# Kernel tuning notes

Hardware: AMD Instinct MI355X
Metric: run time of the kernel (lower is better)

Reference implementation:

```python
import jax, jax.numpy as jnp
import numpy as np

HEADS = 4
DIM_HEAD = 32
IN_CHANNELS = 256
SCALE = DIM_HEAD ** -0.5
EPS = 1e-5


def setup_inputs() -> dict:
    key = jax.random.key(0)
    ks = jax.random.split(key, 6)
    B, C, H, W = 16, IN_CHANNELS, 64, 64
    inner = HEADS * DIM_HEAD  # 128
    x = jax.random.normal(ks[0], (B, C, H, W), dtype=jnp.float32)
    # 1x1 conv weights are [out_ch, in_ch] (kernel spatial dims are 1)
    w_qkv = jax.random.normal(ks[1], (3 * inner, C), dtype=jnp.float32) * (C ** -0.5)
    w_out = jax.random.normal(ks[2], (C, inner), dtype=jnp.float32) * (inner ** -0.5)
    b_out = jax.random.normal(ks[3], (C,), dtype=jnp.float32) * 0.01
    gn_gamma = jnp.ones((C,), dtype=jnp.float32)
    gn_beta = jnp.zeros((C,), dtype=jnp.float32)
    return {"x": x, "w_qkv": w_qkv, "w_out": w_out, "b_out": b_out,
            "gn_gamma": gn_gamma, "gn_beta": gn_beta}


def reference(x, w_qkv, w_out, b_out, gn_gamma, gn_beta):
    b, c, h, w = x.shape
    n = h * w
    inner = HEADS * DIM_HEAD
    # 1x1 conv (no bias): [b, 3*inner, h, w], then chunk into q,k,v along channels
    qkv = jnp.einsum('oc,bchw->bohw', w_qkv, x)
    qkv = qkv.reshape(b, 3, HEADS, DIM_HEAD, n)  # chunk + 'b (h c) x y -> b h c (x y)'
    q, k, v = qkv[:, 0], qkv[:, 1], qkv[:, 2]    # each [b, heads, dim_head, n]
    q = jax.nn.softmax(q, axis=-2) * SCALE       # softmax over dim_head axis
    k = jax.nn.softmax(k, axis=-1)               # softmax over spatial axis
    context = jnp.einsum('bhdn,bhen->bhde', k, v)  # [b, heads, d, e]
    out = jnp.einsum('bhde,bhdn->bhen', context, q)  # [b, heads, e, n]
    out = out.reshape(b, inner, h, w)            # 'b h c (x y) -> b (h c) x y'
    # out 1x1 conv with bias
    out = jnp.einsum('oc,bchw->bohw', w_out, out) + b_out[None, :, None, None]
    # GroupNorm(num_groups=1): normalize over (C,H,W) per sample, per-channel affine
    mean = jnp.mean(out, axis=(1, 2, 3), keepdims=True)
    var = jnp.var(out, axis=(1, 2, 3), keepdims=True)
    out = (out - mean) * jax.lax.rsqrt(var + EPS)
    return out * gn_gamma[None, :, None, None] + gn_beta[None, :, None, None]
```

## Files before the change

### kernel.cpp

```cpp
#include <hip/hip_runtime.h>
#include <hip/hip_bf16.h>
#include <math.h>

#define B_SZ 16
#define C_IN 256
#define HEADS 4
#define DHEAD 32
#define INNER 128
#define QKV_CH 384
#define N_PIX 4096
#define SCALE_Q 0.17677669529663687f
#define GN_EPS 1e-5f
#define NCHK 32

typedef __attribute__((ext_vector_type(8))) short s16x8;
typedef __attribute__((ext_vector_type(4))) float f32x4;
typedef __attribute__((ext_vector_type(8))) unsigned short u16x8;
typedef __attribute__((ext_vector_type(4))) unsigned short u16x4;

__device__ __forceinline__ float waveSum(float v) {
#pragma unroll
  for (int off = 32; off > 0; off >>= 1) v += __shfl_down(v, off, 64);
  return v;
}
__device__ __forceinline__ unsigned short f2bf(float f) {
  unsigned int u = __builtin_bit_cast(unsigned int, f);
  unsigned int r = 0x7FFFu + ((u >> 16) & 1u);
  return (unsigned short)((u + r) >> 16);
}
__device__ __forceinline__ float bf2f(unsigned short u) {
  unsigned int x = ((unsigned int)u) << 16;
  return __builtin_bit_cast(float, x);
}

__global__ __launch_bounds__(256) void cvt_w(const float* __restrict__ wq,
                                             const float* __restrict__ wo,
                                             unsigned short* __restrict__ wqb,
                                             unsigned short* __restrict__ wob) {
  const int i = blockIdx.x * 256 + threadIdx.x;
  if (i < QKV_CH * C_IN) wqb[i] = f2bf(wq[i]);
  if (i < C_IN * INNER) wob[i] = f2bf(wo[i]);
}

__global__ __launch_bounds__(256) void qkv_gemm(const unsigned short* __restrict__ A,
                                                const float* __restrict__ X,
                                                unsigned short* __restrict__ Out) {
  const int b = blockIdx.y;
  const int n0 = blockIdx.x * 128;
  const int tid = threadIdx.x;
  const int w = tid >> 6, l = tid & 63;
  const int lr = l & 15, kg = l >> 4;
  const int mOff = (w >> 1) * 64, nOff = (w & 1) * 64;

  __shared__ unsigned short As[8192];
  __shared__ unsigned short Bs[32768];

  const float* xb = X + (size_t)b * C_IN * N_PIX;
  const int cq = tid >> 4, nq = tid & 15;

  for (int kc = 0; kc < C_IN; kc += 64) {
    float xr[8][4];
#pragma unroll
    for (int ci = 0; ci < 4; ++ci) {
      const float* xp = xb + (size_t)(kc + cq * 4 + ci) * N_PIX + n0 + nq;
#pragma unroll
      for (int k = 0; k < 8; ++k) xr[k][ci] = xp[k * 16];
    }
    const int c0b = (kc + cq * 4) * 2;
#pragma unroll
    for (int k = 0; k < 8; ++k) {
      const int row = nq + k * 16;
      u16x4 w4;
#pragma unroll
      for (int ci = 0; ci < 4; ++ci) w4[ci] = f2bf(xr[k][ci]);
      *reinterpret_cast<u16x4*>((char*)Bs + row * 512 + (c0b ^ ((row & 7) << 4))) = w4;
    }
  }

  unsigned short* Ob = Out + (size_t)b * QKV_CH * N_PIX;

  for (int mt = 0; mt < 3; ++mt) {
    const int m0 = mt * 128;
    f32x4 acc[4][4] = {};
    for (int kc = 0; kc < C_IN; kc += 64) {
#pragma unroll
      for (int s = 0; s < 4; ++s) {
        const int blk = (w * 4 + s) * 64 + l;
        const int r = blk >> 3;
        const int c = ((blk & 7) ^ (r & 7)) << 3;
        __builtin_amdgcn_global_load_lds(
            (const __attribute__((address_space(1))) void*)(A + (size_t)(m0 + r) * C_IN + kc + c),
            (__attribute__((address_space(3))) void*)((char*)As + (w * 4 + s) * 1024), 16, 0, 0);
      }
      __syncthreads();
#pragma unroll
      for (int ks = 0; ks < 2; ++ks) {
        const int kbyteA = ks * 64 + kg * 16;
        const int kbyteB = (kc + ks * 32 + kg * 8) * 2;
        s16x8 av[4], bv[4];
#pragma unroll
        for (int i = 0; i < 4; ++i) {
          const int row = mOff + i * 16 + lr;
          av[i] = *reinterpret_cast<const s16x8*>(
              (const char*)As + row * 128 + (kbyteA ^ ((row & 7) << 4)));
        }
#pragma unroll
        for (int j = 0; j < 4; ++j) {
          const int row = nOff + j * 16 + lr;
          bv[j] = *reinterpret_cast<const s16x8*>(
              (const char*)Bs + row * 512 + (kbyteB ^ ((row & 7) << 4)));
        }
#pragma unroll
        for (int i = 0; i < 4; ++i)
#pragma unroll
          for (int j = 0; j < 4; ++j)
            acc[i][j] = __builtin_amdgcn_mfma_f32_16x16x32_bf16(av[i], bv[j], acc[i][j], 0, 0, 0);
      }
      __syncthreads();
    }
#pragma unroll
    for (int i = 0; i < 4; ++i) {
      const int rowb = m0 + mOff + i * 16 + kg * 4;
#pragma unroll
      for (int j = 0; j < 4; ++j) {
        const int col = n0 + nOff + j * 16 + lr;
#pragma unroll
        for (int r = 0; r < 4; ++r)
          Ob[(size_t)(rowb + r) * N_PIX + col] = f2bf(acc[i][j][r]);
      }
    }
  }
}

__global__ __launch_bounds__(256) void ctx_mfma(const unsigned short* __restrict__ qkv,
                                                float* __restrict__ ctxp,
                                                float* __restrict__ mpart,
                                                float* __restrict__ spart) {
  const int wid = blockIdx.x * 4 + (threadIdx.x >> 6);
  const int l = threadIdx.x & 63;
  const int b = wid >> 7;
  const int h = (wid >> 5) & 3;
  const int c = wid & 31;
  const int lr = l & 15, kg = l >> 4;
  const unsigned short* kb =
      qkv + ((size_t)b * QKV_CH + INNER + h * DHEAD) * N_PIX + c * 128 + kg * 8;
  const unsigned short* vb = kb + (size_t)INNER * N_PIX;

  u16x8 kf[2][4], vf[2][4];
#pragma unroll
  for (int dt = 0; dt < 2; ++dt)
#pragma unroll
    for (int ks = 0; ks < 4; ++ks) {
      kf[dt][ks] = *reinterpret_cast<const u16x8*>(kb + (size_t)(dt * 16 + lr) * N_PIX + ks * 32);
      vf[dt][ks] = *reinterpret_cast<const u16x8*>(vb + (size_t)(dt * 16 + lr) * N_PIX + ks * 32);
    }
  float kv[2][4][8];
  float m[2] = {-INFINITY, -INFINITY};
#pragma unroll
  for (int dt = 0; dt < 2; ++dt)
#pragma unroll
    for (int ks = 0; ks < 4; ++ks)
#pragma unroll
      for (int j = 0; j < 8; ++j) {
        kv[dt][ks][j] = bf2f(kf[dt][ks][j]);
        m[dt] = fmaxf(m[dt], kv[dt][ks][j]);
      }
#pragma unroll
  for (int dt = 0; dt < 2; ++dt) {
    m[dt] = fmaxf(m[dt], __shfl_xor(m[dt], 16, 64));
    m[dt] = fmaxf(m[dt], __shfl_xor(m[dt], 32, 64));
  }
  float s[2] = {0.f, 0.f};
  s16x8 ka[2][4];
#pragma unroll
  for (int dt = 0; dt < 2; ++dt)
#pragma unroll
    for (int ks = 0; ks < 4; ++ks)
#pragma unroll
      for (int j = 0; j < 8; ++j) {
        const float e = __expf(kv[dt][ks][j] - m[dt]);
        s[dt] += e;
        ka[dt][ks][j] = (short)f2bf(e);
      }
#pragma unroll
  for (int dt = 0; dt < 2; ++dt) {
    s[dt] += __shfl_xor(s[dt], 16, 64);
    s[dt] += __shfl_xor(s[dt], 32, 64);
  }
  f32x4 acc[2][2] = {};
#pragma unroll
  for (int ks = 0; ks < 4; ++ks)
#pragma unroll
    for (int dt = 0; dt < 2; ++dt)
#pragma unroll
      for (int et = 0; et < 2; ++et)
        acc[dt][et] = __builtin_amdgcn_mfma_f32_16x16x32_bf16(
            ka[dt][ks], __builtin_bit_cast(s16x8, vf[et][ks]), acc[dt][et], 0, 0, 0);

  float* cp = ctxp + (size_t)wid * 1024;
#pragma unroll
  for (int dt = 0; dt < 2; ++dt)
#pragma unroll
    for (int et = 0; et < 2; ++et)
#pragma unroll
      for (int r = 0; r < 4; ++r)
        cp[(dt * 16 + kg * 4 + r) * 32 + et * 16 + lr] = acc[dt][et][r];
  if (kg == 0) {
    mpart[wid * 32 + lr] = m[0];
    mpart[wid * 32 + 16 + lr] = m[1];
    spart[wid * 32 + lr] = s[0];
    spart[wid * 32 + 16 + lr] = s[1];
  }
}

__global__ __launch_bounds__(256) void ctx_reduce(const float* __restrict__ ctxp,
                                                  const float* __restrict__ mpart,
                                                  const float* __restrict__ spart,
                                                  float* __restrict__ ctxf) {
  const int bh = blockIdx.x;
  const int tid = threadIdx.x;
  __shared__ float ms[NCHK][32], ss[NCHK][32], fac[NCHK][32];
  __shared__ float inv_l[32];
#pragma unroll
  for (int i = 0; i < 4; ++i) {
    const int idx = tid + i * 256;
    ms[idx >> 5][idx & 31] = mpart[(size_t)bh * 1024 + idx];
    ss[idx >> 5][idx & 31] = spart[(size_t)bh * 1024 + idx];
  }
  __syncthreads();
  if (tid < 32) {
    const int d = tid;
    float M = -INFINITY;
    for (int c = 0; c < NCHK; ++c) M = fmaxf(M, ms[c][d]);
    float den = 0.f;
    for (int c = 0; c < NCHK; ++c) {
      const float f = __expf(ms[c][d] - M);
      fac[c][d] = f;
      den += f * ss[c][d];
    }
    inv_l[d] = 1.0f / den;
  }
  __syncthreads();
  const float* cp = ctxp + (size_t)bh * (NCHK * 1024);
#pragma unroll
  for (int i = 0; i < 4; ++i) {
    const int idx = tid + i * 256;
    const int d = idx >> 5;
    float a = 0.f;
    for (int c = 0; c < NCHK; ++c) a += fac[c][d] * cp[(size_t)c * 1024 + idx];
    ctxf[(size_t)bh * 1024 + idx] = a * inv_l[d];
  }
}

__global__ __launch_bounds__(256) void weff_k(const unsigned short* __restrict__ wo,
                                              const float* __restrict__ ctxf,
                                              unsigned short* __restrict__ weff) {
  const int b = blockIdx.z, h = blockIdx.y, oq = blockIdx.x;
  const int tid = threadIdx.x;
  const int o = oq * 64 + (tid >> 2);
  const int d0 = (tid & 3) * 8;

  float wr[32];
  const unsigned short* wp = wo + (size_t)o * INNER + h * DHEAD;
#pragma unroll
  for (int e8 = 0; e8 < 4; ++e8) {
    u16x8 v = *reinterpret_cast<const u16x8*>(wp + e8 * 8);
#pragma unroll
    for (int j = 0; j < 8; ++j) wr[e8 * 8 + j] = bf2f(v[j]);
  }
  const float* cb = ctxf + (size_t)(b * HEADS + h) * 1024;
  u16x8 outv;
#pragma unroll
  for (int dd = 0; dd < 8; ++dd) {
    const float* cr = cb + (size_t)(d0 + dd) * 32;
    float acc = 0.f;
#pragma unroll
    for (int e4 = 0; e4 < 8; ++e4) {
      const f32x4 c4 = *reinterpret_cast<const f32x4*>(cr + e4 * 4);
#pragma unroll
      for (int j = 0; j < 4; ++j) acc += wr[e4 * 4 + j] * c4[j];
    }
    outv[dd] = f2bf(acc);
  }
  unsigned short* op = weff + ((size_t)b * C_IN + o) * INNER + h * DHEAD + d0;
  *reinterpret_cast<u16x8*>(op) = outv;
}

__global__ __launch_bounds__(256) void q_softmax(const unsigned short* __restrict__ qkv,
                                                 unsigned short* __restrict__ qsm_t) {
  const int b = blockIdx.z, h = blockIdx.y;
  const int n = blockIdx.x * 256 + threadIdx.x;
  const unsigned short* qb = qkv + ((size_t)b * QKV_CH + h * DHEAD) * N_PIX + n;
  float q[32];
  float m = -INFINITY;
#pragma unroll
  for (int d2 = 0; d2 < 32; ++d2) {
    q[d2] = bf2f(qb[(size_t)d2 * N_PIX]);
    m = fmaxf(m, q[d2]);
  }
  float s = 0.f;
#pragma unroll
  for (int d2 = 0; d2 < 32; ++d2) {
    q[d2] = __expf(q[d2] - m);
    s += q[d2];
  }
  const float inv = SCALE_Q / s;
  unsigned short* ob = qsm_t + ((size_t)b * N_PIX + n) * INNER + h * DHEAD;
#pragma unroll
  for (int d8 = 0; d8 < 4; ++d8) {
    u16x8 pk;
#pragma unroll
    for (int r = 0; r < 8; ++r) pk[r] = f2bf(q[d8 * 8 + r] * inv);
    *reinterpret_cast<u16x8*>(&ob[d8 * 8]) = pk;
  }
}

template <bool WRITE>
__global__ __launch_bounds__(256) void out_gemm_t(
    const unsigned short* __restrict__ A, const unsigned short* __restrict__ Bm,
    float* __restrict__ Out, const float* __restrict__ bias,
    float* __restrict__ gn_part, const float* __restrict__ gamma,
    const float* __restrict__ beta) {
  const int b = blockIdx.z;
  const int m0 = blockIdx.y * 128;
  const int n0 = blockIdx.x * 128;
  const int tid = threadIdx.x;
  const int w = tid >> 6, l = tid & 63;
  const int lr = l & 15, kg = l >> 4;
  const int mOff = (w >> 1) * 64, nOff = (w & 1) * 64;

  __shared__ unsigned short As[8192];
  __shared__ unsigned short Bs[8192];
  __shared__ float red[8];

  const unsigned short* Ab = A + (size_t)b * C_IN * INNER;
  const unsigned short* Bb = Bm + (size_t)b * N_PIX * INNER;
  f32x4 acc[4][4] = {};

  for (int kc = 0; kc < INNER; kc += 64) {
#pragma unroll
    for (int s = 0; s < 4; ++s) {
      const int blk = (w * 4 + s) * 64 + l;
      const int r = blk >> 3;
      const int c = ((blk & 7) ^ (r & 7)) << 3;
      __builtin_amdgcn_global_load_lds(
          (const __attribute__((address_space(1))) void*)(Ab + (size_t)(m0 + r) * INNER + kc + c),
          (__attribute__((address_space(3))) void*)((char*)As + (w * 4 + s) * 1024), 16, 0, 0);
      __builtin_amdgcn_global_load_lds(
          (const __attribute__((address_space(1))) void*)(Bb + (size_t)(n0 + r) * INNER + kc + c),
          (__attribute__((address_space(3))) void*)((char*)Bs + (w * 4 + s) * 1024), 16, 0, 0);
    }
    __syncthreads();
#pragma unroll
    for (int ks = 0; ks < 2; ++ks) {
      const int kbyte = ks * 64 + kg * 16;
      s16x8 av[4], bv[4];
#pragma unroll
      for (int i = 0; i < 4; ++i) {
        const int row = mOff + i * 16 + lr;
        av[i] = *reinterpret_cast<const s16x8*>(
            (const char*)As + row * 128 + (kbyte ^ ((row & 7) << 4)));
      }
#pragma unroll
      for (int j = 0; j < 4; ++j) {
        const int row = nOff + j * 16 + lr;
        bv[j] = *reinterpret_cast<const s16x8*>(
            (const char*)Bs + row * 128 + (kbyte ^ ((row & 7) << 4)));
      }
#pragma unroll
      for (int i = 0; i < 4; ++i)
#pragma unroll
        for (int j = 0; j < 4; ++j)
          acc[i][j] = __builtin_amdgcn_mfma_f32_16x16x32_bf16(av[i], bv[j], acc[i][j], 0, 0, 0);
    }
    __syncthreads();
  }

  if (!WRITE) {
    float s = 0.f, s2 = 0.f;
#pragma unroll
    for (int i = 0; i < 4; ++i) {
      const int rowb = m0 + mOff + i * 16 + kg * 4;
#pragma unroll
      for (int r = 0; r < 4; ++r) {
        const float bvs = bias[rowb + r];
#pragma unroll
        for (int j = 0; j < 4; ++j) {
          const float v = acc[i][j][r] + bvs;
          s += v;
          s2 += v * v;
        }
      }
    }
    const float S = waveSum(s), S2 = waveSum(s2);
    if (l == 0) {
      red[w] = S;
      red[4 + w] = S2;
    }
    __syncthreads();
    if (tid == 0) {
      const int bid = (b * 2 + blockIdx.y) * 32 + blockIdx.x;
      gn_part[(size_t)bid * 2 + 0] = red[0] + red[1] + red[2] + red[3];
      gn_part[(size_t)bid * 2 + 1] = red[4] + red[5] + red[6] + red[7];
    }
  } else {
    const int i64 = tid & 63;
    float ps = gn_part[(size_t)(b * 64 + i64) * 2 + 0];
    float ps2 = gn_part[(size_t)(b * 64 + i64) * 2 + 1];
    ps = waveSum(ps);
    ps2 = waveSum(ps2);
    const float invn = 1.0f / (float)(C_IN * N_PIX);
    const float mean = __shfl(ps, 0, 64) * invn;
    const float var = __shfl(ps2, 0, 64) * invn - mean * mean;
    const float istd = rsqrtf(var + GN_EPS);

    float* Ob = Out + (size_t)b * C_IN * N_PIX;
#pragma unroll
    for (int i = 0; i < 4; ++i) {
      const int rowb = m0 + mOff + i * 16 + kg * 4;
#pragma unroll
      for (int r = 0; r < 4; ++r) {
        const int ch = rowb + r;
        const float bvs = bias[ch];
        const float g = gamma[ch] * istd;
        const float be = beta[ch];
#pragma unroll
        for (int j = 0; j < 4; ++j) {
          const int col = n0 + nOff + j * 16 + lr;
          const float v = acc[i][j][r] + bvs;
          Ob[(size_t)ch * N_PIX + col] = (v - mean) * g + be;
        }
      }
    }
  }
}

extern "C" void kernel_launch(void* const* d_in, const int* in_sizes, int n_in,
                              void* d_out, int out_size, void* d_ws, size_t ws_size,
                              hipStream_t stream) {
  const float* x = (const float*)d_in[0];
  const float* w_qkv = (const float*)d_in[1];
  const float* w_out = (const float*)d_in[2];
  const float* b_out = (const float*)d_in[3];
  const float* gamma = (const float*)d_in[4];
  const float* beta = (const float*)d_in[5];
  float* out = (float*)d_out;

  char* p = (char*)d_ws;
  unsigned short* qkv_bf = (unsigned short*)p; p += (size_t)B_SZ * QKV_CH * N_PIX * 2;
  unsigned short* qsm_t = (unsigned short*)p;  p += (size_t)B_SZ * N_PIX * INNER * 2;
  unsigned short* wq_bf = (unsigned short*)p;  p += (size_t)QKV_CH * C_IN * 2;
  unsigned short* wo_bf = (unsigned short*)p;  p += (size_t)C_IN * INNER * 2;
  float* ctxp = (float*)p;    p += (size_t)B_SZ * HEADS * NCHK * 1024 * 4;
  float* mpart = (float*)p;   p += (size_t)B_SZ * HEADS * NCHK * 32 * 4;
  float* spart = (float*)p;   p += (size_t)B_SZ * HEADS * NCHK * 32 * 4;
  float* ctxf = (float*)p;    p += (size_t)B_SZ * HEADS * 1024 * 4;
  unsigned short* weff = (unsigned short*)p; p += (size_t)B_SZ * C_IN * INNER * 2;
  float* gn_part = (float*)p; p += (size_t)1024 * 2 * 4;

  cvt_w<<<dim3(384), 256, 0, stream>>>(w_qkv, w_out, wq_bf, wo_bf);
  qkv_gemm<<<dim3(32, B_SZ), 256, 0, stream>>>(wq_bf, x, qkv_bf);
  ctx_mfma<<<dim3(512), 256, 0, stream>>>(qkv_bf, ctxp, mpart, spart);
  ctx_reduce<<<dim3(64), 256, 0, stream>>>(ctxp, mpart, spart, ctxf);
  weff_k<<<dim3(4, HEADS, B_SZ), 256, 0, stream>>>(wo_bf, ctxf, weff);
  q_softmax<<<dim3(16, HEADS, B_SZ), 256, 0, stream>>>(qkv_bf, qsm_t);
  out_gemm_t<false><<<dim3(32, 2, B_SZ), 256, 0, stream>>>(
      weff, qsm_t, nullptr, b_out, gn_part, nullptr, nullptr);
  out_gemm_t<true><<<dim3(32, 2, B_SZ), 256, 0, stream>>>(
      weff, qsm_t, out, b_out, gn_part, gamma, beta);
}
```

Measured before the change: 97.67 us.

## Restructure QKV GEMM into software-pipelined 512-thread kernel with double-buffered X tiles

Rewrites the QKV projection GEMM to use 512-thread blocks over 64-pixel tiles, splitting the 384 output channels into two 192-row halves that each keep accumulators in registers. The X tile is loaded per K-chunk into a double-buffered LDS region and converted to bf16, while weight chunks are fetched with global_load_lds ahead of use. Manual vmcnt/lgkmcnt waits and barriers overlap global loads with MFMA work. The old version staged the whole K range of X first and looped three M tiles. The new schedule doubles the grid and raises per-block LDS to 64KB, which may limit occupancy, and it depends on hand-counted wait thresholds being correct.

Result: no change. 98.91 us (+1.3%).

```diff
diff --git a/kernel.cpp b/kernel.cpp
--- a/kernel.cpp
+++ b/kernel.cpp
@@ -42,94 +42,129 @@
   if (i < C_IN * INNER) wob[i] = f2bf(wo[i]);
 }
 
-__global__ __launch_bounds__(256) void qkv_gemm(const unsigned short* __restrict__ A,
-                                                const float* __restrict__ X,
-                                                unsigned short* __restrict__ Out) {
+__global__ __launch_bounds__(512, 4) void qkv_gemm(const unsigned short* __restrict__ A,
+                                                   const float* __restrict__ X,
+                                                   unsigned short* __restrict__ Out) {
   const int b = blockIdx.y;
-  const int n0 = blockIdx.x * 128;
+  const int n0 = blockIdx.x * 64;
   const int tid = threadIdx.x;
   const int w = tid >> 6, l = tid & 63;
   const int lr = l & 15, kg = l >> 4;
-  const int mOff = (w >> 1) * 64, nOff = (w & 1) * 64;
-
-  __shared__ unsigned short As[8192];
-  __shared__ unsigned short Bs[32768];
+  const int wm = w >> 1, wn = w & 1;
+
+  __shared__ char lds[65536];
+  char* As = lds;
+  char* Bs = lds + 49152;
 
   const float* xb = X + (size_t)b * C_IN * N_PIX;
-  const int cq = tid >> 4, nq = tid & 15;
-
-  for (int kc = 0; kc < C_IN; kc += 64) {
-    float xr[8][4];
-#pragma unroll
-    for (int ci = 0; ci < 4; ++ci) {
-      const float* xp = xb + (size_t)(kc + cq * 4 + ci) * N_PIX + n0 + nq;
-#pragma unroll
-      for (int k = 0; k < 8; ++k) xr[k][ci] = xp[k * 16];
-    }
-    const int c0b = (kc + cq * 4) * 2;
-#pragma unroll
-    for (int k = 0; k < 8; ++k) {
-      const int row = nq + k * 16;
-      u16x4 w4;
-#pragma unroll
-      for (int ci = 0; ci < 4; ++ci) w4[ci] = f2bf(xr[k][ci]);
-      *reinterpret_cast<u16x4*>((char*)Bs + row * 512 + (c0b ^ ((row & 7) << 4))) = w4;
-    }
+  const int c_loc = ((tid >> 3) & 7) + w * 8;
+  const int oct = tid & 7;
+
+  auto ISSUE_A = [&](int kc, int half) {
+#pragma unroll
+    for (int it = 0; it < 3; ++it) {
+      const int idx = it * 512 + tid;
+      const int r = idx >> 3;
+      const int srcb = ((idx & 7) << 4) ^ ((r & 7) << 4);
+      __builtin_amdgcn_global_load_lds(
+          (const __attribute__((address_space(1))) void*)((const char*)A +
+              ((size_t)(half * 192 + r) * C_IN + kc * 64) * 2 + srcb),
+          (__attribute__((address_space(3))) void*)(As + half * 24576 + idx * 16), 16, 0, 0);
+    }
+  };
+
+  f32x4 xr0, xr1;
+  auto ISSUE_X = [&](int kc) {
+    const float* xp = xb + (size_t)(kc * 64 + c_loc) * N_PIX + n0 + oct * 8;
+    xr0 = *reinterpret_cast<const f32x4*>(xp);
+    xr1 = *reinterpret_cast<const f32x4*>(xp + 4);
+  };
+
+  auto WRITE_B = [&](int pb) {
+#pragma unroll
+    for (int j = 0; j < 8; ++j) {
+      const int n = oct * 8 + j;
+      const float v = (j < 4) ? xr0[j] : xr1[j - 4];
+      *reinterpret_cast<unsigned short*>(
+          Bs + pb * 8192 + n * 128 + ((2 * c_loc) ^ (((n ^ (n >> 3)) & 7) << 4))) = f2bf(v);
+    }
+  };
+
+  f32x4 acc[2][3][2] = {};
+
+  auto COMPUTE = [&](int kc, int half) {
+    const char* Ab = As + half * 24576;
+    const char* Bb = Bs + (kc & 1) * 8192;
+#pragma unroll
+    for (int ks = 0; ks < 2; ++ks) {
+      const int kb = ks * 64 + kg * 16;
+      s16x8 av[3], bv[2];
+#pragma unroll
+      for (int i = 0; i < 3; ++i) {
+        const int r = wm * 48 + i * 16 + lr;
+        av[i] = *reinterpret_cast<const s16x8*>(Ab + r * 128 + (kb ^ ((r & 7) << 4)));
+      }
+#pragma unroll
+      for (int j = 0; j < 2; ++j) {
+        const int n = wn * 32 + j * 16 + lr;
+        bv[j] = *reinterpret_cast<const s16x8*>(Bb + n * 128 +
+                                                (kb ^ (((n ^ (n >> 3)) & 7) << 4)));
+      }
+#pragma unroll
+      for (int i = 0; i < 3; ++i)
+#pragma unroll
+        for (int j = 0; j < 2; ++j)
+          acc[half][i][j] =
+              __builtin_amdgcn_mfma_f32_16x16x32_bf16(av[i], bv[j], acc[half][i][j], 0, 0, 0);
+    }
+  };
+
+  ISSUE_A(0, 0);
+  ISSUE_X(0);
+  asm volatile("s_waitcnt vmcnt(0)" ::: "memory");
+  WRITE_B(0);
+  asm volatile("s_waitcnt lgkmcnt(0)" ::: "memory");
+  __builtin_amdgcn_s_barrier();
+
+  for (int kc = 0; kc < 4; ++kc) {
+    ISSUE_A(kc, 1);
+    if (kc < 3) {
+      ISSUE_X(kc + 1);
+      asm volatile("s_waitcnt vmcnt(5)" ::: "memory");
+    } else {
+      asm volatile("s_waitcnt vmcnt(3)" ::: "memory");
+    }
+    __builtin_amdgcn_s_barrier();
+    COMPUTE(kc, 0);
+    asm volatile("s_waitcnt lgkmcnt(0)" ::: "memory");
+    __builtin_amdgcn_s_barrier();
+    if (kc < 3) {
+      ISSUE_A(kc + 1, 0);
+      asm volatile("s_waitcnt vmcnt(3)" ::: "memory");
+    } else {
+      asm volatile("s_waitcnt vmcnt(0)" ::: "memory");
+    }
+    __builtin_amdgcn_s_barrier();
+    if (kc < 3) WRITE_B((kc + 1) & 1);
+    COMPUTE(kc, 1);
+    asm volatile("s_waitcnt lgkmcnt(0)" ::: "memory");
+    __builtin_amdgcn_s_barrier();
   }
 
   unsigned short* Ob = Out + (size_t)b * QKV_CH * N_PIX;
-
-  for (int mt = 0; mt < 3; ++mt) {
-    const int m0 = mt * 128;
-    f32x4 acc[4][4] = {};
-    for (int kc = 0; kc < C_IN; kc += 64) {
-#pragma unroll
-      for (int s = 0; s < 4; ++s) {
-        const int blk = (w * 4 + s) * 64 + l;
-        const int r = blk >> 3;
-        const int c = ((blk & 7) ^ (r & 7)) << 3;
-        __builtin_amdgcn_global_load_lds(
-            (const __attribute__((address_space(1))) void*)(A + (size_t)(m0 + r) * C_IN + kc + c),
-            (__attribute__((address_space(3))) void*)((char*)As + (w * 4 + s) * 1024), 16, 0, 0);
-      }
-      __syncthreads();
-#pragma unroll
-      for (int ks = 0; ks < 2; ++ks) {
-        const int kbyteA = ks * 64 + kg * 16;
-        const int kbyteB = (kc + ks * 32 + kg * 8) * 2;
-        s16x8 av[4], bv[4];
-#pragma unroll
-        for (int i = 0; i < 4; ++i) {
-          const int row = mOff + i * 16 + lr;
-          av[i] = *reinterpret_cast<const s16x8*>(
-              (const char*)As + row * 128 + (kbyteA ^ ((row & 7) << 4)));
-        }
-#pragma unroll
-        for (int j = 0; j < 4; ++j) {
-          const int row = nOff + j * 16 + lr;
-          bv[j] = *reinterpret_cast<const s16x8*>(
-              (const char*)Bs + row * 512 + (kbyteB ^ ((row & 7) << 4)));
-        }
-#pragma unroll
-        for (int i = 0; i < 4; ++i)
-#pragma unroll
-          for (int j = 0; j < 4; ++j)
-            acc[i][j] = __builtin_amdgcn_mfma_f32_16x16x32_bf16(av[i], bv[j], acc[i][j], 0, 0, 0);
-      }
-      __syncthreads();
-    }
-#pragma unroll
-    for (int i = 0; i < 4; ++i) {
-      const int rowb = m0 + mOff + i * 16 + kg * 4;
-#pragma unroll
-      for (int j = 0; j < 4; ++j) {
-        const int col = n0 + nOff + j * 16 + lr;
+#pragma unroll
+  for (int half = 0; half < 2; ++half)
+#pragma unroll
+    for (int i = 0; i < 3; ++i) {
+      const int mrow = half * 192 + wm * 48 + i * 16 + kg * 4;
+#pragma unroll
+      for (int j = 0; j < 2; ++j) {
+        const int col = n0 + wn * 32 + j * 16 + lr;
 #pragma unroll
         for (int r = 0; r < 4; ++r)
-          Ob[(size_t)(rowb + r) * N_PIX + col] = f2bf(acc[i][j][r]);
-      }
-    }
-  }
+          Ob[(size_t)(mrow + r) * N_PIX + col] = f2bf(acc[half][i][j][r]);
+      }
+    }
 }
 
 __global__ __launch_bounds__(256) void ctx_mfma(const unsigned short* __restrict__ qkv,
@@ -459,7 +494,7 @@
   float* gn_part = (float*)p; p += (size_t)1024 * 2 * 4;
 
   cvt_w<<<dim3(384), 256, 0, stream>>>(w_qkv, w_out, wq_bf, wo_bf);
-  qkv_gemm<<<dim3(32, B_SZ), 256, 0, stream>>>(wq_bf, x, qkv_bf);
+  qkv_gemm<<<dim3(64, B_SZ), 512, 0, stream>>>(wq_bf, x, qkv_bf);
   ctx_mfma<<<dim3(512), 256, 0, stream>>>(qkv_bf, ctxp, mpart, spart);
   ctx_reduce<<<dim3(64), 256, 0, stream>>>(ctxp, mpart, spart, ctxf);
   weff_k<<<dim3(4, HEADS, B_SZ), 256, 0, stream>>>(wo_bf, ctxf, weff);
```
